# Kernel optimization log

Measured on AMD Instinct MI355X. Metric: run time of the kernel, lower is better.

The kernel has to match this reference:

```python
import jax, jax.numpy as jnp
import numpy as np

B, T = 64, 512
VOCAB = 1024
HID = [512, 512]
STATE = HID[0]          # 512
CELL_IN = 2 * STATE     # 1024 (emb || h)
CELL_OUT = STATE + VOCAB  # 1536
SKIP_DIM = sum(HID)     # 1024


def setup_inputs() -> dict:
    key = jax.random.key(0)
    ks = jax.random.split(key, 8)
    s = 0.02
    x = jax.random.randint(ks[0], (B, T), 0, VOCAB, dtype=jnp.int32)
    emb = jax.random.normal(ks[1], (VOCAB, STATE), dtype=jnp.float32) * s
    W0 = jax.random.normal(ks[2], (CELL_IN, HID[0]), dtype=jnp.float32) * s
    b0 = jnp.zeros((HID[0],), dtype=jnp.float32)
    W1 = jax.random.normal(ks[3], (HID[0], HID[1]), dtype=jnp.float32) * s
    b1 = jnp.zeros((HID[1],), dtype=jnp.float32)
    Wout = jax.random.normal(ks[4], (SKIP_DIM, CELL_OUT), dtype=jnp.float32) * s
    bout = jnp.zeros((CELL_OUT,), dtype=jnp.float32)
    return {"x": x, "emb": emb, "W0": W0, "b0": b0, "W1": W1, "b1": b1,
            "Wout": Wout, "bout": bout}


def reference(x, emb, W0, b0, W1, b1, Wout, bout):
    # embedding gather for all timesteps: [B, T, STATE] -> [T, B, STATE] for scan
    e = emb[x].transpose(1, 0, 2)

    def step(h, e_t):
        inp = jnp.concatenate([e_t, h], axis=-1)          # [B, 2*STATE]
        h0 = jax.nn.relu(inp @ W0 + b0)                   # [B, HID0]
        h1 = jax.nn.relu(h0 @ W1 + b1)                    # [B, HID1]
        cat = jnp.concatenate([h0, h1], axis=-1)          # skip connection
        cell_out = cat @ Wout + bout                      # [B, STATE+VOCAB]
        h_new = jax.nn.relu(cell_out[:, :STATE])
        logits = cell_out[:, STATE:]
        return h_new, logits

    h0 = jnp.zeros((x.shape[0], STATE), dtype=emb.dtype)
    _, logits = jax.lax.scan(step, h0, e)                 # logits: [T, B, VOCAB]
    return logits.transpose(1, 0, 2)                      # [B, T, VOCAB]
```

## Files before the change

### kernel.cpp

```cpp
#include <hip/hip_runtime.h>
#include <hip/hip_bf16.h>

typedef __attribute__((ext_vector_type(8))) short short8;
typedef __attribute__((ext_vector_type(4))) float f32x4;
typedef __attribute__((ext_vector_type(2))) unsigned long long u64x2;

#define MFMA16(a, b, c) __builtin_amdgcn_mfma_f32_16x16x32_bf16((a), (b), (c), 0, 0, 0)

#define B_ 64
#define T_ 512
#define STATE_ 512
#define NG 16
#define NGROUPS 4

#define CNT_OFF   0u
#define HBUF_OFF  24576u
#define CAT_OFF   155648u
#define W0F_OFF   67264512u
#define W1F_OFF   68313088u
#define WAF_OFF   68837376u
#define WBT_OFF   69885952u

__device__ __forceinline__ short f2bf(float f) {
  unsigned u = __float_as_uint(f);
  unsigned r = (u + 0x7fffu + ((u >> 16) & 1u)) >> 16;
  return (short)r;
}

__device__ __forceinline__ short8 ld8(const short* p) {
  union { u64x2 q; short8 s; } u;
  u.q.x = __hip_atomic_load((const unsigned long long*)p, __ATOMIC_RELAXED, __HIP_MEMORY_SCOPE_AGENT);
  u.q.y = __hip_atomic_load(((const unsigned long long*)p) + 1, __ATOMIC_RELAXED, __HIP_MEMORY_SCOPE_AGENT);
  return u.s;
}

__device__ __forceinline__ void st2(short* p, float v0, float v1) {
  unsigned pk = ((unsigned)(unsigned short)f2bf(v1) << 16) | (unsigned)(unsigned short)f2bf(v0);
  __hip_atomic_store((unsigned*)p, pk, __ATOMIC_RELAXED, __HIP_MEMORY_SCOPE_AGENT);
}

__global__ void pack_weights(const float* __restrict__ W0, const float* __restrict__ W1,
                             const float* __restrict__ Wout,
                             short* __restrict__ W0f, short* __restrict__ W1f,
                             short* __restrict__ Waf, short* __restrict__ WbT) {
  const int total = 524288 + 262144 + 524288 + 1048576;
  for (int i = blockIdx.x * blockDim.x + threadIdx.x; i < total; i += gridDim.x * blockDim.x) {
    if (i < 524288) {
      int j = i & 7, l = (i >> 3) & 63, rest = i >> 9;
      int s = rest & 31, cb = rest >> 5;
      int k = s * 32 + ((l >> 4) << 3) + j, n = (cb << 4) + (l & 15);
      W0f[i] = f2bf(W0[k * 512 + n]);
    } else if (i < 786432) {
      int ii = i - 524288;
      int j = ii & 7, l = (ii >> 3) & 63, rest = ii >> 9;
      int s = rest & 15, cb = rest >> 4;
      int k = s * 32 + ((l >> 4) << 3) + j, n = (cb << 4) + (l & 15);
      W1f[ii] = f2bf(W1[k * 512 + n]);
    } else if (i < 1310720) {
      int ii = i - 786432;
      int j = ii & 7, l = (ii >> 3) & 63, rest = ii >> 9;
      int s = rest & 31, cb = rest >> 5;
      int k = s * 32 + ((l >> 4) << 3) + j, n = (cb << 4) + (l & 15);
      Waf[ii] = f2bf(Wout[k * 1536 + n]);
    } else {
      int ii = i - 1310720;
      int v = ii >> 10, k = ii & 1023;
      WbT[ii] = f2bf(Wout[k * 1536 + 512 + v]);
    }
  }
}

__device__ __forceinline__ void group_barrier(unsigned* __restrict__ flags, int g, int m,
                                              unsigned tag) {
  __syncthreads();
  const int tid = threadIdx.x;
  if (tid == 0)
    __hip_atomic_store(&flags[(g << 4) + m], tag, __ATOMIC_RELEASE, __HIP_MEMORY_SCOPE_AGENT);
  if (tid < NG) {
    int spins = 0;
    while (__hip_atomic_load(&flags[(g << 4) + tid], __ATOMIC_RELAXED,
                             __HIP_MEMORY_SCOPE_AGENT) < tag) {
      if (++spins > (1 << 16)) break;
    }
  }
  __syncthreads();
}

__device__ __forceinline__ float rsum(const float* red, int rr, int col) {
  int o = ((col >> 4) << 8) + rr * 16 + (col & 15);
  return red[o] + red[o + 512] + red[o + 1024] + red[o + 1536];
}

__global__ __launch_bounds__(256, 1) void rnn_recur(
    const int* __restrict__ x, const float* __restrict__ emb,
    const float* __restrict__ b0, const float* __restrict__ b1,
    const float* __restrict__ bout,
    const short* __restrict__ W0f, const short* __restrict__ W1f,
    const short* __restrict__ Waf,
    short* __restrict__ cat, short* __restrict__ hbuf, unsigned* __restrict__ flags) {
  const int tid = threadIdx.x;
  const int l = tid & 63, w = tid >> 6;
  const int g = blockIdx.x >> 4, m = blockIdx.x & 15;
  const int rowbase = g << 4, colbase = m << 5;
  __shared__ float red[2048];

  short8 w0f[2][8], waL[2][4], waH[2][4], w1f[2][4];
#pragma unroll
  for (int tile = 0; tile < 2; ++tile) {
    int cb = m * 2 + tile;
#pragma unroll
    for (int s = 0; s < 8; ++s)
      w0f[tile][s] = *(const short8*)&W0f[((cb * 32 + w * 8 + s) * 64 + l) * 8];
#pragma unroll
    for (int s = 0; s < 4; ++s) {
      waL[tile][s] = *(const short8*)&Waf[((cb * 32 + w * 4 + s) * 64 + l) * 8];
      waH[tile][s] = *(const short8*)&Waf[((cb * 32 + 16 + w * 4 + s) * 64 + l) * 8];
      w1f[tile][s] = *(const short8*)&W1f[((cb * 16 + w * 4 + s) * 64 + l) * 8];
    }
  }

  const int cp = tid & 15, rr2 = tid >> 4;
  const float b0a = b0[colbase + 2 * cp],   b0b = b0[colbase + 2 * cp + 1];
  const float b1a = b1[colbase + 2 * cp],   b1b = b1[colbase + 2 * cp + 1];
  const float bOa = bout[colbase + 2 * cp], bOb = bout[colbase + 2 * cp + 1];

  const int myrow = rowbase + (l & 15);
  const int kgrp = (l >> 4) * 8;

  for (int t = 0; t < T_; ++t) {
    {
      f32x4 acc0 = {0.f, 0.f, 0.f, 0.f}, acc1 = {0.f, 0.f, 0.f, 0.f};
      if (w < 2) {
        int idx = x[myrow * T_ + t];
        const float* erow = emb + (long)idx * STATE_ + w * 256 + kgrp;
#pragma unroll
        for (int s = 0; s < 8; ++s) {
          const float* p = erow + s * 32;
          short8 a;
#pragma unroll
          for (int j = 0; j < 8; ++j) a[j] = f2bf(p[j]);
          acc0 = MFMA16(a, w0f[0][s], acc0);
          acc1 = MFMA16(a, w0f[1][s], acc1);
        }
      } else {
        const short* hrow = hbuf + ((t & 1) << 15) + (myrow << 9) + (w - 2) * 256 + kgrp;
#pragma unroll
        for (int s = 0; s < 8; ++s) {
          short8 a = ld8(hrow + s * 32);
          acc0 = MFMA16(a, w0f[0][s], acc0);
          acc1 = MFMA16(a, w0f[1][s], acc1);
        }
      }
#pragma unroll
      for (int j = 0; j < 4; ++j) {
        red[w * 512 +       ((l >> 4) * 4 + j) * 16 + (l & 15)] = acc0[j];
        red[w * 512 + 256 + ((l >> 4) * 4 + j) * 16 + (l & 15)] = acc1[j];
      }
      __syncthreads();
      float v0 = fmaxf(rsum(red, rr2, 2 * cp) + b0a, 0.f);
      float v1 = fmaxf(rsum(red, rr2, 2 * cp + 1) + b0b, 0.f);
      st2(&cat[(t * B_ + rowbase + rr2) * 1024 + colbase + 2 * cp], v0, v1);
    }
    group_barrier(flags, g, m, (unsigned)(t * 3 + 1));

    f32x4 accP0 = {0.f, 0.f, 0.f, 0.f}, accP1 = {0.f, 0.f, 0.f, 0.f};
    {
      f32x4 acc0 = {0.f, 0.f, 0.f, 0.f}, acc1 = {0.f, 0.f, 0.f, 0.f};
      const short* crow = cat + (t * B_ + myrow) * 1024 + w * 128 + kgrp;
#pragma unroll
      for (int s = 0; s < 4; ++s) {
        short8 a = ld8(crow + s * 32);
        acc0 = MFMA16(a, w1f[0][s], acc0);
        acc1 = MFMA16(a, w1f[1][s], acc1);
        accP0 = MFMA16(a, waL[0][s], accP0);
        accP1 = MFMA16(a, waL[1][s], accP1);
      }
#pragma unroll
      for (int j = 0; j < 4; ++j) {
        red[w * 512 +       ((l >> 4) * 4 + j) * 16 + (l & 15)] = acc0[j];
        red[w * 512 + 256 + ((l >> 4) * 4 + j) * 16 + (l & 15)] = acc1[j];
      }
      __syncthreads();
      float v0 = fmaxf(rsum(red, rr2, 2 * cp) + b1a, 0.f);
      float v1 = fmaxf(rsum(red, rr2, 2 * cp + 1) + b1b, 0.f);
      st2(&cat[(t * B_ + rowbase + rr2) * 1024 + 512 + colbase + 2 * cp], v0, v1);
    }
    if (t == T_ - 1) break;
    group_barrier(flags, g, m, (unsigned)(t * 3 + 2));

    {
      const short* crow = cat + (t * B_ + myrow) * 1024 + 512 + w * 128 + kgrp;
#pragma unroll
      for (int s = 0; s < 4; ++s) {
        short8 a = ld8(crow + s * 32);
        accP0 = MFMA16(a, waH[0][s], accP0);
        accP1 = MFMA16(a, waH[1][s], accP1);
      }
#pragma unroll
      for (int j = 0; j < 4; ++j) {
        red[w * 512 +       ((l >> 4) * 4 + j) * 16 + (l & 15)] = accP0[j];
        red[w * 512 + 256 + ((l >> 4) * 4 + j) * 16 + (l & 15)] = accP1[j];
      }
      __syncthreads();
      float v0 = fmaxf(rsum(red, rr2, 2 * cp) + bOa, 0.f);
      float v1 = fmaxf(rsum(red, rr2, 2 * cp + 1) + bOb, 0.f);
      st2(&hbuf[(((t + 1) & 1) << 15) + (rowbase + rr2) * 512 + colbase + 2 * cp], v0, v1);
    }
    group_barrier(flags, g, m, (unsigned)(t * 3 + 3));
  }
}

__global__ __launch_bounds__(256) void logits_gemm(const short* __restrict__ cat,
                                                   const short* __restrict__ WbT,
                                                   const float* __restrict__ bout,
                                                   float* __restrict__ out) {
  const int mbase = (blockIdx.x >> 3) * 128;
  const int vbase = (blockIdx.x & 7) * 128;
  __shared__ short sA[128 * 32];
  __shared__ short sB[128 * 32];
  const int tid = threadIdx.x, l = tid & 63, w = tid >> 6;
  const int wm = w & 1, wn = w >> 1;

  f32x4 acc[4][4];
#pragma unroll
  for (int i = 0; i < 4; ++i)
#pragma unroll
    for (int j = 0; j < 4; ++j) acc[i][j] = (f32x4){0.f, 0.f, 0.f, 0.f};

  for (int kb = 0; kb < 1024; kb += 32) {
    __syncthreads();
#pragma unroll
    for (int it = 0; it < 2; ++it) {
      int c = tid + 256 * it;
      int ml = c >> 2, ks = c & 3;
      *(short8*)&sA[ml * 32 + ks * 8] = *(const short8*)&cat[(mbase + ml) * 1024 + kb + ks * 8];
      *(short8*)&sB[ml * 32 + ks * 8] = *(const short8*)&WbT[(vbase + ml) * 1024 + kb + ks * 8];
    }
    __syncthreads();
    short8 af[4], bf[4];
#pragma unroll
    for (int fr = 0; fr < 4; ++fr)
      af[fr] = *(const short8*)&sA[(wm * 64 + fr * 16 + (l & 15)) * 32 + (l >> 4) * 8];
#pragma unroll
    for (int fc = 0; fc < 4; ++fc)
      bf[fc] = *(const short8*)&sB[(wn * 64 + fc * 16 + (l & 15)) * 32 + (l >> 4) * 8];
#pragma unroll
    for (int fr = 0; fr < 4; ++fr)
#pragma unroll
      for (int fc = 0; fc < 4; ++fc) acc[fr][fc] = MFMA16(af[fr], bf[fc], acc[fr][fc]);
  }

  float bb[4];
#pragma unroll
  for (int fc = 0; fc < 4; ++fc) bb[fc] = bout[512 + vbase + wn * 64 + fc * 16 + (l & 15)];

#pragma unroll
  for (int fr = 0; fr < 4; ++fr) {
#pragma unroll
    for (int fc = 0; fc < 4; ++fc) {
      int v = vbase + wn * 64 + fc * 16 + (l & 15);
#pragma unroll
      for (int j = 0; j < 4; ++j) {
        int mm = mbase + wm * 64 + fr * 16 + (l >> 4) * 4 + j;
        int b = mm & 63, tt = mm >> 6;
        out[((long)(b * T_ + tt)) * 1024 + v] = acc[fr][fc][j] + bb[fc];
      }
    }
  }
}

extern "C" void kernel_launch(void* const* d_in, const int* in_sizes, int n_in,
                              void* d_out, int out_size, void* d_ws, size_t ws_size,
                              hipStream_t stream) {
  const int*   x    = (const int*)d_in[0];
  const float* emb  = (const float*)d_in[1];
  const float* W0   = (const float*)d_in[2];
  const float* b0   = (const float*)d_in[3];
  const float* W1   = (const float*)d_in[4];
  const float* b1   = (const float*)d_in[5];
  const float* Wout = (const float*)d_in[6];
  const float* bout = (const float*)d_in[7];
  float* out = (float*)d_out;

  char* ws = (char*)d_ws;
  unsigned* flags = (unsigned*)(ws + CNT_OFF);
  short* hbuf = (short*)(ws + HBUF_OFF);
  short* cat  = (short*)(ws + CAT_OFF);
  short* W0f  = (short*)(ws + W0F_OFF);
  short* W1f  = (short*)(ws + W1F_OFF);
  short* Waf  = (short*)(ws + WAF_OFF);
  short* WbT  = (short*)(ws + WBT_OFF);

  hipMemsetAsync(ws, 0, HBUF_OFF + 131072u, stream);
  pack_weights<<<1024, 256, 0, stream>>>(W0, W1, Wout, W0f, W1f, Waf, WbT);
  rnn_recur<<<64, 256, 0, stream>>>(x, emb, b0, b1, bout, W0f, W1f, Waf, cat, hbuf, flags);
  logits_gemm<<<2048, 256, 0, stream>>>(cat, WbT, bout, out);
}
```

Baseline: 6.368 ms.

## Remap recurrent blocks onto XCDs with full-K per wave and per-XCD flag barriers

Each block now reads its XCC id at startup and claims a slot so that each group of 8 batch rows runs on 8 blocks sharing one XCD. Each wave owns a 16-column tile over the full K dimension, so the LDS cross-wave reduction and its syncthreads go away. Barriers become split signal/wait flags, and when a group fits on one XCD it uses plain loads and stores without cache invalidation. The embedding is pre-converted to bf16 and the token ids are staged in LDS. In exchange it holds far more weights in registers and depends on an XCC-placement rendezvous among all 64 blocks.

```diff
diff --git a/kernel.cpp b/kernel.cpp
--- a/kernel.cpp
+++ b/kernel.cpp
@@ -9,17 +9,16 @@
 
 #define B_ 64
 #define T_ 512
-#define STATE_ 512
-#define NG 16
-#define NGROUPS 4
-
-#define CNT_OFF   0u
-#define HBUF_OFF  24576u
-#define CAT_OFF   155648u
-#define W0F_OFF   67264512u
-#define W1F_OFF   68313088u
-#define WAF_OFF   68837376u
-#define WBT_OFF   69885952u
+
+#define ORG_OFF   0u
+#define FLAGS_OFF 1024u
+#define HBUF_OFF  4096u
+#define CAT_OFF   135168u
+#define W0F_OFF   67244032u
+#define W1F_OFF   68292608u
+#define WAF_OFF   68816896u
+#define WBT_OFF   69865472u
+#define EMBF_OFF  71962624u
 
 __device__ __forceinline__ short f2bf(float f) {
   unsigned u = __float_as_uint(f);
@@ -34,16 +33,22 @@
   return u.s;
 }
 
-__device__ __forceinline__ void st2(short* p, float v0, float v1) {
-  unsigned pk = ((unsigned)(unsigned short)f2bf(v1) << 16) | (unsigned)(unsigned short)f2bf(v0);
-  __hip_atomic_store((unsigned*)p, pk, __ATOMIC_RELAXED, __HIP_MEMORY_SCOPE_AGENT);
+__device__ __forceinline__ void st_bf(short* p, float v, int fast) {
+  unsigned short b = (unsigned short)f2bf(v);
+  if (fast) {
+    *p = (short)b;
+  } else {
+    unsigned vv = b;
+    asm volatile("global_store_short %0, %1, off sc0 sc1" :: "v"(p), "v"(vv) : "memory");
+  }
 }
 
 __global__ void pack_weights(const float* __restrict__ W0, const float* __restrict__ W1,
-                             const float* __restrict__ Wout,
+                             const float* __restrict__ Wout, const float* __restrict__ emb,
                              short* __restrict__ W0f, short* __restrict__ W1f,
-                             short* __restrict__ Waf, short* __restrict__ WbT) {
-  const int total = 524288 + 262144 + 524288 + 1048576;
+                             short* __restrict__ Waf, short* __restrict__ WbT,
+                             short* __restrict__ embf) {
+  const int total = 524288 + 262144 + 524288 + 1048576 + 524288;
   for (int i = blockIdx.x * blockDim.x + threadIdx.x; i < total; i += gridDim.x * blockDim.x) {
     if (i < 524288) {
       int j = i & 7, l = (i >> 3) & 63, rest = i >> 9;
@@ -62,151 +67,185 @@
       int s = rest & 31, cb = rest >> 5;
       int k = s * 32 + ((l >> 4) << 3) + j, n = (cb << 4) + (l & 15);
       Waf[ii] = f2bf(Wout[k * 1536 + n]);
-    } else {
+    } else if (i < 2359296) {
       int ii = i - 1310720;
       int v = ii >> 10, k = ii & 1023;
       WbT[ii] = f2bf(Wout[k * 1536 + 512 + v]);
-    }
-  }
-}
-
-__device__ __forceinline__ void group_barrier(unsigned* __restrict__ flags, int g, int m,
-                                              unsigned tag) {
+    } else {
+      int ii = i - 2359296;
+      embf[ii] = f2bf(emb[ii]);
+    }
+  }
+}
+
+__device__ __forceinline__ void wait_tag(unsigned* gf, unsigned tag, int inv) {
+  if (threadIdx.x < 8) {
+    int spins = 0;
+    while (__hip_atomic_load(&gf[threadIdx.x], __ATOMIC_RELAXED, __HIP_MEMORY_SCOPE_AGENT) < tag) {
+      if (++spins > (1 << 22)) break;
+    }
+  }
   __syncthreads();
-  const int tid = threadIdx.x;
-  if (tid == 0)
-    __hip_atomic_store(&flags[(g << 4) + m], tag, __ATOMIC_RELEASE, __HIP_MEMORY_SCOPE_AGENT);
-  if (tid < NG) {
-    int spins = 0;
-    while (__hip_atomic_load(&flags[(g << 4) + tid], __ATOMIC_RELAXED,
-                             __HIP_MEMORY_SCOPE_AGENT) < tag) {
-      if (++spins > (1 << 16)) break;
-    }
-  }
+  if (inv) asm volatile("buffer_inv" ::: "memory");
+}
+
+__device__ __forceinline__ void signal_tag(unsigned* gf, int mb, unsigned tag) {
   __syncthreads();
-}
-
-__device__ __forceinline__ float rsum(const float* red, int rr, int col) {
-  int o = ((col >> 4) << 8) + rr * 16 + (col & 15);
-  return red[o] + red[o + 512] + red[o + 1024] + red[o + 1536];
+  if (threadIdx.x == 0) {
+    asm volatile("" ::: "memory");
+    __hip_atomic_store(&gf[mb], tag, __ATOMIC_RELAXED, __HIP_MEMORY_SCOPE_AGENT);
+  }
 }
 
 __global__ __launch_bounds__(256, 1) void rnn_recur(
-    const int* __restrict__ x, const float* __restrict__ emb,
-    const float* __restrict__ b0, const float* __restrict__ b1,
-    const float* __restrict__ bout,
-    const short* __restrict__ W0f, const short* __restrict__ W1f,
-    const short* __restrict__ Waf,
-    short* __restrict__ cat, short* __restrict__ hbuf, unsigned* __restrict__ flags) {
+    const int* __restrict__ x,
+    const float* __restrict__ b0, const float* __restrict__ b1, const float* __restrict__ bout,
+    const short* __restrict__ W0f, const short* __restrict__ W1f, const short* __restrict__ Waf,
+    const short* __restrict__ embf,
+    short* __restrict__ cat, short* __restrict__ hbuf,
+    unsigned* __restrict__ org, unsigned* __restrict__ flagsbase) {
   const int tid = threadIdx.x;
   const int l = tid & 63, w = tid >> 6;
-  const int g = blockIdx.x >> 4, m = blockIdx.x & 15;
-  const int rowbase = g << 4, colbase = m << 5;
-  __shared__ float red[2048];
-
-  short8 w0f[2][8], waL[2][4], waH[2][4], w1f[2][4];
-#pragma unroll
-  for (int tile = 0; tile < 2; ++tile) {
-    int cb = m * 2 + tile;
-#pragma unroll
-    for (int s = 0; s < 8; ++s)
-      w0f[tile][s] = *(const short8*)&W0f[((cb * 32 + w * 8 + s) * 64 + l) * 8];
-#pragma unroll
-    for (int s = 0; s < 4; ++s) {
-      waL[tile][s] = *(const short8*)&Waf[((cb * 32 + w * 4 + s) * 64 + l) * 8];
-      waH[tile][s] = *(const short8*)&Waf[((cb * 32 + 16 + w * 4 + s) * 64 + l) * 8];
-      w1f[tile][s] = *(const short8*)&W1f[((cb * 16 + w * 4 + s) * 64 + l) * 8];
-    }
-  }
-
-  const int cp = tid & 15, rr2 = tid >> 4;
-  const float b0a = b0[colbase + 2 * cp],   b0b = b0[colbase + 2 * cp + 1];
-  const float b1a = b1[colbase + 2 * cp],   b1b = b1[colbase + 2 * cp + 1];
-  const float bOa = bout[colbase + 2 * cp], bOb = bout[colbase + 2 * cp + 1];
-
-  const int myrow = rowbase + (l & 15);
-  const int kgrp = (l >> 4) * 8;
+  __shared__ int s_g, s_m, s_fast;
+  __shared__ int x_lds[8][512];
+
+  if (tid == 0) {
+    unsigned xcc = __builtin_amdgcn_s_getreg(20 | (31 << 11)) & 7u;
+    int slot = (int)__hip_atomic_fetch_add(&org[xcc], 1u, __ATOMIC_RELAXED, __HIP_MEMORY_SCOPE_AGENT);
+    int sp = -1;
+    if (slot >= 8)
+      sp = (int)__hip_atomic_fetch_add(&org[8], 1u, __ATOMIC_RELAXED, __HIP_MEMORY_SCOPE_AGENT);
+    __hip_atomic_fetch_add(&org[9], 1u, __ATOMIC_RELEASE, __HIP_MEMORY_SCOPE_AGENT);
+    int spins = 0;
+    while (__hip_atomic_load(&org[9], __ATOMIC_ACQUIRE, __HIP_MEMORY_SCOPE_AGENT) < 64u) {
+      if (++spins > (1 << 22)) break;
+    }
+    unsigned c[8];
+    for (int i = 0; i < 8; ++i)
+      c[i] = __hip_atomic_load(&org[i], __ATOMIC_RELAXED, __HIP_MEMORY_SCOPE_AGENT);
+    int g, mb;
+    if (sp < 0) { g = (int)xcc; mb = slot; }
+    else {
+      int want = sp, acc = 0; g = 0; mb = 0;
+      for (int xx = 0; xx < 8; ++xx) {
+        int d = (c[xx] < 8u) ? (8 - (int)c[xx]) : 0;
+        if (want < acc + d) { g = xx; mb = (int)c[xx] + (want - acc); break; }
+        acc += d;
+      }
+    }
+    s_g = g; s_m = mb; s_fast = (c[g] >= 8u) ? 1 : 0;
+  }
+  __syncthreads();
+  const int g = s_g, mb = s_m, fast = s_fast;
+
+  for (int i = tid; i < 8 * 512; i += 256)
+    x_lds[i >> 9][i & 511] = x[(g * 8 + (i >> 9)) * T_ + (i & 511)];
+
+  const int cb = mb * 4 + w;
+  short8 w0f[32], w1f[16], waf[32];
+#pragma unroll
+  for (int s = 0; s < 32; ++s) w0f[s] = *(const short8*)&W0f[((cb * 32 + s) * 64 + l) * 8];
+#pragma unroll
+  for (int s = 0; s < 16; ++s) w1f[s] = *(const short8*)&W1f[((cb * 16 + s) * 64 + l) * 8];
+#pragma unroll
+  for (int s = 0; s < 32; ++s) waf[s] = *(const short8*)&Waf[((cb * 32 + s) * 64 + l) * 8];
+
+  const int col512 = cb * 16 + (l & 15);
+  const int lrow = (l & 15) & 7;
+  const int kofs = (l >> 4) * 8;
+  const float b0v = b0[col512], b1v = b1[col512], bOv = bout[col512];
+  unsigned* gf = flagsbase + g * 16;
+  __syncthreads();
 
   for (int t = 0; t < T_; ++t) {
-    {
-      f32x4 acc0 = {0.f, 0.f, 0.f, 0.f}, acc1 = {0.f, 0.f, 0.f, 0.f};
-      if (w < 2) {
-        int idx = x[myrow * T_ + t];
-        const float* erow = emb + (long)idx * STATE_ + w * 256 + kgrp;
-#pragma unroll
-        for (int s = 0; s < 8; ++s) {
-          const float* p = erow + s * 32;
-          short8 a;
-#pragma unroll
-          for (int j = 0; j < 8; ++j) a[j] = f2bf(p[j]);
-          acc0 = MFMA16(a, w0f[0][s], acc0);
-          acc1 = MFMA16(a, w0f[1][s], acc1);
+    f32x4 accA = {0.f, 0.f, 0.f, 0.f}, accB = {0.f, 0.f, 0.f, 0.f};
+    {
+      int idx = x_lds[lrow][t];
+      const short* ep = embf + idx * 512 + kofs;
+#pragma unroll
+      for (int s = 0; s < 16; s += 2) {
+        short8 a0 = *(const short8*)(ep + s * 32);
+        short8 a1 = *(const short8*)(ep + s * 32 + 32);
+        accA = MFMA16(a0, w0f[s], accA);
+        accB = MFMA16(a1, w0f[s + 1], accB);
+      }
+    }
+    wait_tag(gf, (unsigned)(3 * t), fast);
+    {
+      const short* hp = hbuf + ((t & 1) << 15) + ((g * 8 + lrow) << 9) + kofs;
+      if (fast) {
+#pragma unroll
+        for (int s = 0; s < 16; s += 2) {
+          short8 a0 = *(const short8*)(hp + s * 32);
+          short8 a1 = *(const short8*)(hp + s * 32 + 32);
+          accA = MFMA16(a0, w0f[16 + s], accA);
+          accB = MFMA16(a1, w0f[17 + s], accB);
         }
       } else {
-        const short* hrow = hbuf + ((t & 1) << 15) + (myrow << 9) + (w - 2) * 256 + kgrp;
-#pragma unroll
-        for (int s = 0; s < 8; ++s) {
-          short8 a = ld8(hrow + s * 32);
-          acc0 = MFMA16(a, w0f[0][s], acc0);
-          acc1 = MFMA16(a, w0f[1][s], acc1);
+#pragma unroll
+        for (int s = 0; s < 16; s += 2) {
+          short8 a0 = ld8(hp + s * 32);
+          short8 a1 = ld8(hp + s * 32 + 32);
+          accA = MFMA16(a0, w0f[16 + s], accA);
+          accB = MFMA16(a1, w0f[17 + s], accB);
         }
       }
+    }
+    {
+      f32x4 hv = accA + accB;
+      short* cp = cat + (t * B_ + g * 8) * 1024 + col512;
 #pragma unroll
       for (int j = 0; j < 4; ++j) {
-        red[w * 512 +       ((l >> 4) * 4 + j) * 16 + (l & 15)] = acc0[j];
-        red[w * 512 + 256 + ((l >> 4) * 4 + j) * 16 + (l & 15)] = acc1[j];
-      }
-      __syncthreads();
-      float v0 = fmaxf(rsum(red, rr2, 2 * cp) + b0a, 0.f);
-      float v1 = fmaxf(rsum(red, rr2, 2 * cp + 1) + b0b, 0.f);
-      st2(&cat[(t * B_ + rowbase + rr2) * 1024 + colbase + 2 * cp], v0, v1);
-    }
-    group_barrier(flags, g, m, (unsigned)(t * 3 + 1));
-
-    f32x4 accP0 = {0.f, 0.f, 0.f, 0.f}, accP1 = {0.f, 0.f, 0.f, 0.f};
-    {
-      f32x4 acc0 = {0.f, 0.f, 0.f, 0.f}, acc1 = {0.f, 0.f, 0.f, 0.f};
-      const short* crow = cat + (t * B_ + myrow) * 1024 + w * 128 + kgrp;
-#pragma unroll
-      for (int s = 0; s < 4; ++s) {
-        short8 a = ld8(crow + s * 32);
-        acc0 = MFMA16(a, w1f[0][s], acc0);
-        acc1 = MFMA16(a, w1f[1][s], acc1);
-        accP0 = MFMA16(a, waL[0][s], accP0);
-        accP1 = MFMA16(a, waL[1][s], accP1);
-      }
+        int r = (l >> 4) * 4 + j;
+        if (r < 8) st_bf(cp + r * 1024, fmaxf(hv[j] + b0v, 0.f), fast);
+      }
+    }
+    signal_tag(gf, mb, (unsigned)(3 * t + 1));
+
+    wait_tag(gf, (unsigned)(3 * t + 1), 0);
+    f32x4 pA = {0.f, 0.f, 0.f, 0.f}, pB = {0.f, 0.f, 0.f, 0.f};
+    {
+      f32x4 hA = {0.f, 0.f, 0.f, 0.f}, hB = {0.f, 0.f, 0.f, 0.f};
+      const short* c0 = cat + (t * B_ + g * 8 + lrow) * 1024 + kofs;
+#pragma unroll
+      for (int s = 0; s < 16; s += 2) {
+        short8 a0 = *(const short8*)(c0 + s * 32);
+        short8 a1 = *(const short8*)(c0 + s * 32 + 32);
+        hA = MFMA16(a0, w1f[s], hA);
+        hB = MFMA16(a1, w1f[s + 1], hB);
+        pA = MFMA16(a0, waf[s], pA);
+        pB = MFMA16(a1, waf[s + 1], pB);
+      }
+      f32x4 hv = hA + hB;
+      short* cp = cat + (t * B_ + g * 8) * 1024 + 512 + col512;
 #pragma unroll
       for (int j = 0; j < 4; ++j) {
-        red[w * 512 +       ((l >> 4) * 4 + j) * 16 + (l & 15)] = acc0[j];
-        red[w * 512 + 256 + ((l >> 4) * 4 + j) * 16 + (l & 15)] = acc1[j];
-      }
-      __syncthreads();
-      float v0 = fmaxf(rsum(red, rr2, 2 * cp) + b1a, 0.f);
-      float v1 = fmaxf(rsum(red, rr2, 2 * cp + 1) + b1b, 0.f);
-      st2(&cat[(t * B_ + rowbase + rr2) * 1024 + 512 + colbase + 2 * cp], v0, v1);
+        int r = (l >> 4) * 4 + j;
+        if (r < 8) st_bf(cp + r * 1024, fmaxf(hv[j] + b1v, 0.f), fast);
+      }
     }
     if (t == T_ - 1) break;
-    group_barrier(flags, g, m, (unsigned)(t * 3 + 2));
-
-    {
-      const short* crow = cat + (t * B_ + myrow) * 1024 + 512 + w * 128 + kgrp;
-#pragma unroll
-      for (int s = 0; s < 4; ++s) {
-        short8 a = ld8(crow + s * 32);
-        accP0 = MFMA16(a, waH[0][s], accP0);
-        accP1 = MFMA16(a, waH[1][s], accP1);
-      }
+    signal_tag(gf, mb, (unsigned)(3 * t + 2));
+
+    wait_tag(gf, (unsigned)(3 * t + 2), 0);
+    {
+      const short* c1 = cat + (t * B_ + g * 8 + lrow) * 1024 + 512 + kofs;
+#pragma unroll
+      for (int s = 0; s < 16; s += 2) {
+        short8 a0 = *(const short8*)(c1 + s * 32);
+        short8 a1 = *(const short8*)(c1 + s * 32 + 32);
+        pA = MFMA16(a0, waf[16 + s], pA);
+        pB = MFMA16(a1, waf[17 + s], pB);
+      }
+      f32x4 hv = pA + pB;
+      short* hq = hbuf + (((t + 1) & 1) << 15) + (g * 8) * 512 + col512;
 #pragma unroll
       for (int j = 0; j < 4; ++j) {
-        red[w * 512 +       ((l >> 4) * 4 + j) * 16 + (l & 15)] = accP0[j];
-        red[w * 512 + 256 + ((l >> 4) * 4 + j) * 16 + (l & 15)] = accP1[j];
-      }
-      __syncthreads();
-      float v0 = fmaxf(rsum(red, rr2, 2 * cp) + bOa, 0.f);
-      float v1 = fmaxf(rsum(red, rr2, 2 * cp + 1) + bOb, 0.f);
-      st2(&hbuf[(((t + 1) & 1) << 15) + (rowbase + rr2) * 512 + colbase + 2 * cp], v0, v1);
-    }
-    group_barrier(flags, g, m, (unsigned)(t * 3 + 3));
+        int r = (l >> 4) * 4 + j;
+        if (r < 8) st_bf(hq + r * 512, fmaxf(hv[j] + bOv, 0.f), fast);
+      }
+    }
+    signal_tag(gf, mb, (unsigned)(3 * t + 3));
   }
 }
 
@@ -283,16 +322,18 @@
   float* out = (float*)d_out;
 
   char* ws = (char*)d_ws;
-  unsigned* flags = (unsigned*)(ws + CNT_OFF);
+  unsigned* org   = (unsigned*)(ws + ORG_OFF);
+  unsigned* flags = (unsigned*)(ws + FLAGS_OFF);
   short* hbuf = (short*)(ws + HBUF_OFF);
   short* cat  = (short*)(ws + CAT_OFF);
   short* W0f  = (short*)(ws + W0F_OFF);
   short* W1f  = (short*)(ws + W1F_OFF);
   short* Waf  = (short*)(ws + WAF_OFF);
   short* WbT  = (short*)(ws + WBT_OFF);
+  short* embf = (short*)(ws + EMBF_OFF);
 
   hipMemsetAsync(ws, 0, HBUF_OFF + 131072u, stream);
-  pack_weights<<<1024, 256, 0, stream>>>(W0, W1, Wout, W0f, W1f, Waf, WbT);
-  rnn_recur<<<64, 256, 0, stream>>>(x, emb, b0, b1, bout, W0f, W1f, Waf, cat, hbuf, flags);
+  pack_weights<<<1024, 256, 0, stream>>>(W0, W1, Wout, emb, W0f, W1f, Waf, WbT, embf);
+  rnn_recur<<<64, 256, 0, stream>>>(x, b0, b1, bout, W0f, W1f, Waf, embf, cat, hbuf, org, flags);
   logits_gemm<<<2048, 256, 0, stream>>>(cat, WbT, bout, out);
 }
```

Result: no change. 6.426 ms (+0.9%).

## Precompute embedding projection and restructure recurrence to redundant-compute per batch group

Applied to the files above, without the earlier changes.

Adds an eprime kernel that precomputes emb @ W0[:512] for the whole vocabulary, so each step only gathers a row instead of multiplying the embedding half. The recurrence now runs 16 blocks of 1024 threads. Each block of four computes h0 and h1 redundantly in LDS from the full h state, then splits only the state-output projection, so there is one cross-block flag sync per step instead of three. This cuts inter-block synchronisation and global round-trips on the serial critical path. In exchange it duplicates the h0/h1 work in every block, uses fewer CUs, and Epr stays in fp32, which changes the rounding point of the embedding term.

```diff
diff --git a/kernel.cpp b/kernel.cpp
--- a/kernel.cpp
+++ b/kernel.cpp
@@ -9,17 +9,15 @@
 
 #define B_ 64
 #define T_ 512
-#define STATE_ 512
-#define NG 16
-#define NGROUPS 4
-
-#define CNT_OFF   0u
-#define HBUF_OFF  24576u
-#define CAT_OFF   155648u
-#define W0F_OFF   67264512u
-#define W1F_OFF   68313088u
-#define WAF_OFF   68837376u
-#define WBT_OFF   69885952u
+
+#define FLG_OFF  0u
+#define HNEW_OFF 1024u
+#define CAT_OFF  66560u
+#define W0F_OFF  67175424u
+#define W1F_OFF  67699712u
+#define WAF_OFF  68224000u
+#define WBT_OFF  69272576u
+#define EPR_OFF  71369728u
 
 __device__ __forceinline__ short f2bf(float f) {
   unsigned u = __float_as_uint(f);
@@ -34,179 +32,271 @@
   return u.s;
 }
 
-__device__ __forceinline__ void st2(short* p, float v0, float v1) {
-  unsigned pk = ((unsigned)(unsigned short)f2bf(v1) << 16) | (unsigned)(unsigned short)f2bf(v0);
-  __hip_atomic_store((unsigned*)p, pk, __ATOMIC_RELAXED, __HIP_MEMORY_SCOPE_AGENT);
-}
-
 __global__ void pack_weights(const float* __restrict__ W0, const float* __restrict__ W1,
                              const float* __restrict__ Wout,
                              short* __restrict__ W0f, short* __restrict__ W1f,
                              short* __restrict__ Waf, short* __restrict__ WbT) {
-  const int total = 524288 + 262144 + 524288 + 1048576;
+  const int total = 262144 + 262144 + 524288 + 1048576;
   for (int i = blockIdx.x * blockDim.x + threadIdx.x; i < total; i += gridDim.x * blockDim.x) {
-    if (i < 524288) {
+    if (i < 262144) {
       int j = i & 7, l = (i >> 3) & 63, rest = i >> 9;
-      int s = rest & 31, cb = rest >> 5;
+      int s = rest & 15, cb = rest >> 4;
       int k = s * 32 + ((l >> 4) << 3) + j, n = (cb << 4) + (l & 15);
-      W0f[i] = f2bf(W0[k * 512 + n]);
-    } else if (i < 786432) {
-      int ii = i - 524288;
+      W0f[i] = f2bf(W0[(512 + k) * 512 + n]);
+    } else if (i < 524288) {
+      int ii = i - 262144;
       int j = ii & 7, l = (ii >> 3) & 63, rest = ii >> 9;
       int s = rest & 15, cb = rest >> 4;
       int k = s * 32 + ((l >> 4) << 3) + j, n = (cb << 4) + (l & 15);
       W1f[ii] = f2bf(W1[k * 512 + n]);
-    } else if (i < 1310720) {
-      int ii = i - 786432;
+    } else if (i < 1048576) {
+      int ii = i - 524288;
       int j = ii & 7, l = (ii >> 3) & 63, rest = ii >> 9;
       int s = rest & 31, cb = rest >> 5;
       int k = s * 32 + ((l >> 4) << 3) + j, n = (cb << 4) + (l & 15);
       Waf[ii] = f2bf(Wout[k * 1536 + n]);
     } else {
-      int ii = i - 1310720;
-      int v = ii >> 10, k = ii & 1023;
-      WbT[ii] = f2bf(Wout[k * 1536 + 512 + v]);
-    }
-  }
-}
-
-__device__ __forceinline__ void group_barrier(unsigned* __restrict__ flags, int g, int m,
-                                              unsigned tag) {
+      int ii = i - 1048576;
+      int v = ii >> 10, kk = ii & 1023;
+      WbT[ii] = f2bf(Wout[kk * 1536 + 512 + v]);
+    }
+  }
+}
+
+__global__ __launch_bounds__(256) void eprime(const float* __restrict__ emb,
+                                              const float* __restrict__ W0,
+                                              float* __restrict__ Epr) {
+  __shared__ float eL[16][512];
+  const int v0 = blockIdx.x * 16, tid = threadIdx.x;
+  for (int i = tid; i < 16 * 512; i += 256)
+    eL[i >> 9][i & 511] = emb[(v0 + (i >> 9)) * 512 + (i & 511)];
   __syncthreads();
-  const int tid = threadIdx.x;
-  if (tid == 0)
-    __hip_atomic_store(&flags[(g << 4) + m], tag, __ATOMIC_RELEASE, __HIP_MEMORY_SCOPE_AGENT);
-  if (tid < NG) {
-    int spins = 0;
-    while (__hip_atomic_load(&flags[(g << 4) + tid], __ATOMIC_RELAXED,
-                             __HIP_MEMORY_SCOPE_AGENT) < tag) {
-      if (++spins > (1 << 16)) break;
-    }
-  }
-  __syncthreads();
-}
-
-__device__ __forceinline__ float rsum(const float* red, int rr, int col) {
-  int o = ((col >> 4) << 8) + rr * 16 + (col & 15);
-  return red[o] + red[o + 512] + red[o + 1024] + red[o + 1536];
-}
-
-__global__ __launch_bounds__(256, 1) void rnn_recur(
-    const int* __restrict__ x, const float* __restrict__ emb,
-    const float* __restrict__ b0, const float* __restrict__ b1,
-    const float* __restrict__ bout,
-    const short* __restrict__ W0f, const short* __restrict__ W1f,
-    const short* __restrict__ Waf,
-    short* __restrict__ cat, short* __restrict__ hbuf, unsigned* __restrict__ flags) {
-  const int tid = threadIdx.x;
-  const int l = tid & 63, w = tid >> 6;
-  const int g = blockIdx.x >> 4, m = blockIdx.x & 15;
-  const int rowbase = g << 4, colbase = m << 5;
-  __shared__ float red[2048];
-
-  short8 w0f[2][8], waL[2][4], waH[2][4], w1f[2][4];
-#pragma unroll
-  for (int tile = 0; tile < 2; ++tile) {
-    int cb = m * 2 + tile;
-#pragma unroll
-    for (int s = 0; s < 8; ++s)
-      w0f[tile][s] = *(const short8*)&W0f[((cb * 32 + w * 8 + s) * 64 + l) * 8];
-#pragma unroll
-    for (int s = 0; s < 4; ++s) {
-      waL[tile][s] = *(const short8*)&Waf[((cb * 32 + w * 4 + s) * 64 + l) * 8];
-      waH[tile][s] = *(const short8*)&Waf[((cb * 32 + 16 + w * 4 + s) * 64 + l) * 8];
-      w1f[tile][s] = *(const short8*)&W1f[((cb * 16 + w * 4 + s) * 64 + l) * 8];
-    }
-  }
-
-  const int cp = tid & 15, rr2 = tid >> 4;
-  const float b0a = b0[colbase + 2 * cp],   b0b = b0[colbase + 2 * cp + 1];
-  const float b1a = b1[colbase + 2 * cp],   b1b = b1[colbase + 2 * cp + 1];
-  const float bOa = bout[colbase + 2 * cp], bOb = bout[colbase + 2 * cp + 1];
-
-  const int myrow = rowbase + (l & 15);
-  const int kgrp = (l >> 4) * 8;
+  float acc[32];
+#pragma unroll
+  for (int v = 0; v < 32; ++v) acc[v] = 0.f;
+#pragma unroll 4
+  for (int k = 0; k < 512; ++k) {
+    float wa = W0[k * 512 + tid];
+    float wb = W0[k * 512 + 256 + tid];
+#pragma unroll
+    for (int v = 0; v < 16; ++v) {
+      float e = eL[v][k];
+      acc[2 * v]     = fmaf(e, wa, acc[2 * v]);
+      acc[2 * v + 1] = fmaf(e, wb, acc[2 * v + 1]);
+    }
+  }
+#pragma unroll
+  for (int v = 0; v < 16; ++v) {
+    Epr[(v0 + v) * 512 + tid]       = acc[2 * v];
+    Epr[(v0 + v) * 512 + 256 + tid] = acc[2 * v + 1];
+  }
+}
+
+__global__ __launch_bounds__(1024, 1) void rnn_recur(
+    const int* __restrict__ x,
+    const float* __restrict__ b0, const float* __restrict__ b1, const float* __restrict__ bout,
+    const short* __restrict__ W0f, const short* __restrict__ W1f, const short* __restrict__ Waf,
+    const float* __restrict__ Epr,
+    short* __restrict__ cat, unsigned* __restrict__ hnewG, unsigned* __restrict__ flags) {
+  const int g = blockIdx.x >> 2, m = blockIdx.x & 3;
+  const int tid = threadIdx.x, l = tid & 63, w = tid >> 6;
+  const int ks = w >> 3, cs = w & 7;
+  const int kq = w >> 2, cw = w & 3;
+  const int q = l >> 4, r16 = l & 15;
+
+  __shared__ short hst[16 * 512];
+  __shared__ short h0s[16 * 512];
+  __shared__ short h1s[16 * 512];
+  __shared__ float part[8][4][16][17];
+  __shared__ float part3[3][4][2][16][17];
+  __shared__ short pub[16 * 128];
+
+  short8 w0r[4][8], w1r[4][8], war[2][8];
+#pragma unroll
+  for (int cb = 0; cb < 4; ++cb) {
+    int cbg = cs * 4 + cb;
+#pragma unroll
+    for (int si = 0; si < 8; ++si) {
+      int s = ks * 8 + si;
+      w0r[cb][si] = *(const short8*)&W0f[((cbg * 16 + s) * 64 + l) * 8];
+      w1r[cb][si] = *(const short8*)&W1f[((cbg * 16 + s) * 64 + l) * 8];
+    }
+  }
+#pragma unroll
+  for (int cb = 0; cb < 2; ++cb) {
+    int cbg = m * 8 + cw * 2 + cb;
+#pragma unroll
+    for (int si = 0; si < 8; ++si) {
+      int s = kq * 8 + si;
+      war[cb][si] = *(const short8*)&Waf[((cbg * 32 + s) * 64 + l) * 8];
+    }
+  }
+
+  float b0v[4], b1v[4];
+#pragma unroll
+  for (int cb = 0; cb < 4; ++cb) {
+    int c = (cs * 4 + cb) * 16 + r16;
+    b0v[cb] = b0[c]; b1v[cb] = b1[c];
+  }
+  float bov[2];
+#pragma unroll
+  for (int cb = 0; cb < 2; ++cb) bov[cb] = bout[(m * 8 + cw * 2 + cb) * 16 + r16];
+
+  float epf[16];
+  if (ks == 1) {
+#pragma unroll
+    for (int j = 0; j < 4; ++j) {
+      int xi = x[(g * 16 + q * 4 + j) * T_ + 0];
+#pragma unroll
+      for (int cb = 0; cb < 4; ++cb)
+        epf[cb * 4 + j] = Epr[xi * 512 + (cs * 4 + cb) * 16 + r16];
+    }
+  }
 
   for (int t = 0; t < T_; ++t) {
+    if (tid < 4) {
+      int spins = 0;
+      while (__hip_atomic_load(&flags[g * 16 + tid], __ATOMIC_RELAXED,
+                               __HIP_MEMORY_SCOPE_AGENT) < (unsigned)t) {
+        if (++spins > (1 << 22)) break;
+      }
+    }
+    __syncthreads();
     {
-      f32x4 acc0 = {0.f, 0.f, 0.f, 0.f}, acc1 = {0.f, 0.f, 0.f, 0.f};
-      if (w < 2) {
-        int idx = x[myrow * T_ + t];
-        const float* erow = emb + (long)idx * STATE_ + w * 256 + kgrp;
-#pragma unroll
-        for (int s = 0; s < 8; ++s) {
-          const float* p = erow + s * 32;
-          short8 a;
-#pragma unroll
-          for (int j = 0; j < 8; ++j) a[j] = f2bf(p[j]);
-          acc0 = MFMA16(a, w0f[0][s], acc0);
-          acc1 = MFMA16(a, w0f[1][s], acc1);
+      short8 hv = ld8((const short*)hnewG + g * 8192 + tid * 8);
+      int rr = tid >> 6, cbyte = (tid & 63) * 16;
+      *(short8*)&hst[rr * 512 + ((cbyte ^ ((rr & 7) << 6)) >> 1)] = hv;
+    }
+    __syncthreads();
+
+    {
+      f32x4 acc[4];
+#pragma unroll
+      for (int cb = 0; cb < 4; ++cb) acc[cb] = (f32x4){0.f, 0.f, 0.f, 0.f};
+#pragma unroll
+      for (int si = 0; si < 8; ++si) {
+        int kbyte = (ks * 256 + si * 32 + q * 8) * 2;
+        short8 af = *(const short8*)&hst[r16 * 512 + ((kbyte ^ ((r16 & 7) << 6)) >> 1)];
+#pragma unroll
+        for (int cb = 0; cb < 4; ++cb) acc[cb] = MFMA16(af, w0r[cb][si], acc[cb]);
+      }
+      if (ks == 0) {
+#pragma unroll
+        for (int cb = 0; cb < 4; ++cb)
+#pragma unroll
+          for (int j = 0; j < 4; ++j) part[cs][cb][q * 4 + j][r16] = acc[cb][j];
+      }
+      __syncthreads();
+      if (ks == 1) {
+#pragma unroll
+        for (int cb = 0; cb < 4; ++cb) {
+          int c = (cs * 4 + cb) * 16 + r16;
+#pragma unroll
+          for (int j = 0; j < 4; ++j) {
+            int rr = q * 4 + j;
+            float v = acc[cb][j] + part[cs][cb][rr][r16] + epf[cb * 4 + j] + b0v[cb];
+            short bf = f2bf(fmaxf(v, 0.f));
+            h0s[rr * 512 + (((c * 2) ^ ((rr & 7) << 6)) >> 1)] = bf;
+            if (m == 0) cat[(t * B_ + g * 16 + rr) * 1024 + c] = bf;
+          }
         }
-      } else {
-        const short* hrow = hbuf + ((t & 1) << 15) + (myrow << 9) + (w - 2) * 256 + kgrp;
-#pragma unroll
-        for (int s = 0; s < 8; ++s) {
-          short8 a = ld8(hrow + s * 32);
-          acc0 = MFMA16(a, w0f[0][s], acc0);
-          acc1 = MFMA16(a, w0f[1][s], acc1);
+      }
+      __syncthreads();
+    }
+
+    {
+      f32x4 acc[4];
+#pragma unroll
+      for (int cb = 0; cb < 4; ++cb) acc[cb] = (f32x4){0.f, 0.f, 0.f, 0.f};
+#pragma unroll
+      for (int si = 0; si < 8; ++si) {
+        int kbyte = (ks * 256 + si * 32 + q * 8) * 2;
+        short8 af = *(const short8*)&h0s[r16 * 512 + ((kbyte ^ ((r16 & 7) << 6)) >> 1)];
+#pragma unroll
+        for (int cb = 0; cb < 4; ++cb) acc[cb] = MFMA16(af, w1r[cb][si], acc[cb]);
+      }
+      if (ks == 0) {
+#pragma unroll
+        for (int cb = 0; cb < 4; ++cb)
+#pragma unroll
+          for (int j = 0; j < 4; ++j) part[cs][cb][q * 4 + j][r16] = acc[cb][j];
+      }
+      __syncthreads();
+      if (ks == 1) {
+#pragma unroll
+        for (int cb = 0; cb < 4; ++cb) {
+          int c = (cs * 4 + cb) * 16 + r16;
+#pragma unroll
+          for (int j = 0; j < 4; ++j) {
+            int rr = q * 4 + j;
+            float v = acc[cb][j] + part[cs][cb][rr][r16] + b1v[cb];
+            short bf = f2bf(fmaxf(v, 0.f));
+            h1s[rr * 512 + (((c * 2) ^ ((rr & 7) << 6)) >> 1)] = bf;
+            if (m == 1) cat[(t * B_ + g * 16 + rr) * 1024 + 512 + c] = bf;
+          }
         }
-      }
-#pragma unroll
-      for (int j = 0; j < 4; ++j) {
-        red[w * 512 +       ((l >> 4) * 4 + j) * 16 + (l & 15)] = acc0[j];
-        red[w * 512 + 256 + ((l >> 4) * 4 + j) * 16 + (l & 15)] = acc1[j];
-      }
-      __syncthreads();
-      float v0 = fmaxf(rsum(red, rr2, 2 * cp) + b0a, 0.f);
-      float v1 = fmaxf(rsum(red, rr2, 2 * cp + 1) + b0b, 0.f);
-      st2(&cat[(t * B_ + rowbase + rr2) * 1024 + colbase + 2 * cp], v0, v1);
-    }
-    group_barrier(flags, g, m, (unsigned)(t * 3 + 1));
-
-    f32x4 accP0 = {0.f, 0.f, 0.f, 0.f}, accP1 = {0.f, 0.f, 0.f, 0.f};
+        if (t + 1 < T_) {
+#pragma unroll
+          for (int j = 0; j < 4; ++j) {
+            int xi = x[(g * 16 + q * 4 + j) * T_ + t + 1];
+#pragma unroll
+            for (int cb = 0; cb < 4; ++cb)
+              epf[cb * 4 + j] = Epr[xi * 512 + (cs * 4 + cb) * 16 + r16];
+          }
+        }
+      }
+      __syncthreads();
+    }
+
+    if (t == T_ - 1) break;
+
     {
-      f32x4 acc0 = {0.f, 0.f, 0.f, 0.f}, acc1 = {0.f, 0.f, 0.f, 0.f};
-      const short* crow = cat + (t * B_ + myrow) * 1024 + w * 128 + kgrp;
-#pragma unroll
-      for (int s = 0; s < 4; ++s) {
-        short8 a = ld8(crow + s * 32);
-        acc0 = MFMA16(a, w1f[0][s], acc0);
-        acc1 = MFMA16(a, w1f[1][s], acc1);
-        accP0 = MFMA16(a, waL[0][s], accP0);
-        accP1 = MFMA16(a, waL[1][s], accP1);
-      }
-#pragma unroll
-      for (int j = 0; j < 4; ++j) {
-        red[w * 512 +       ((l >> 4) * 4 + j) * 16 + (l & 15)] = acc0[j];
-        red[w * 512 + 256 + ((l >> 4) * 4 + j) * 16 + (l & 15)] = acc1[j];
-      }
-      __syncthreads();
-      float v0 = fmaxf(rsum(red, rr2, 2 * cp) + b1a, 0.f);
-      float v1 = fmaxf(rsum(red, rr2, 2 * cp + 1) + b1b, 0.f);
-      st2(&cat[(t * B_ + rowbase + rr2) * 1024 + 512 + colbase + 2 * cp], v0, v1);
-    }
-    if (t == T_ - 1) break;
-    group_barrier(flags, g, m, (unsigned)(t * 3 + 2));
-
-    {
-      const short* crow = cat + (t * B_ + myrow) * 1024 + 512 + w * 128 + kgrp;
-#pragma unroll
-      for (int s = 0; s < 4; ++s) {
-        short8 a = ld8(crow + s * 32);
-        accP0 = MFMA16(a, waH[0][s], accP0);
-        accP1 = MFMA16(a, waH[1][s], accP1);
-      }
-#pragma unroll
-      for (int j = 0; j < 4; ++j) {
-        red[w * 512 +       ((l >> 4) * 4 + j) * 16 + (l & 15)] = accP0[j];
-        red[w * 512 + 256 + ((l >> 4) * 4 + j) * 16 + (l & 15)] = accP1[j];
-      }
-      __syncthreads();
-      float v0 = fmaxf(rsum(red, rr2, 2 * cp) + bOa, 0.f);
-      float v1 = fmaxf(rsum(red, rr2, 2 * cp + 1) + bOb, 0.f);
-      st2(&hbuf[(((t + 1) & 1) << 15) + (rowbase + rr2) * 512 + colbase + 2 * cp], v0, v1);
-    }
-    group_barrier(flags, g, m, (unsigned)(t * 3 + 3));
+      f32x4 a3[2];
+#pragma unroll
+      for (int cb = 0; cb < 2; ++cb) a3[cb] = (f32x4){0.f, 0.f, 0.f, 0.f};
+      const short* src = (kq < 2) ? h0s : h1s;
+      int kb = (kq & 1) * 256;
+#pragma unroll
+      for (int si = 0; si < 8; ++si) {
+        int kbyte = (kb + si * 32 + q * 8) * 2;
+        short8 af = *(const short8*)&src[r16 * 512 + ((kbyte ^ ((r16 & 7) << 6)) >> 1)];
+#pragma unroll
+        for (int cb = 0; cb < 2; ++cb) a3[cb] = MFMA16(af, war[cb][si], a3[cb]);
+      }
+      if (kq < 3) {
+#pragma unroll
+        for (int cb = 0; cb < 2; ++cb)
+#pragma unroll
+          for (int j = 0; j < 4; ++j) part3[kq][cw][cb][q * 4 + j][r16] = a3[cb][j];
+      }
+      __syncthreads();
+      if (kq == 3) {
+#pragma unroll
+        for (int cb = 0; cb < 2; ++cb) {
+          int lc = (cw * 2 + cb) * 16 + r16;
+#pragma unroll
+          for (int j = 0; j < 4; ++j) {
+            int rr = q * 4 + j;
+            float v = a3[cb][j] + part3[0][cw][cb][rr][r16] + part3[1][cw][cb][rr][r16] +
+                      part3[2][cw][cb][rr][r16] + bov[cb];
+            pub[rr * 128 + lc] = f2bf(fmaxf(v, 0.f));
+          }
+        }
+      }
+      __syncthreads();
+      {
+        int rr = tid >> 6, c2 = tid & 63;
+        unsigned word = ((const unsigned*)pub)[rr * 64 + c2];
+        __hip_atomic_store(&hnewG[g * 4096 + rr * 256 + m * 64 + c2], word,
+                           __ATOMIC_RELAXED, __HIP_MEMORY_SCOPE_AGENT);
+      }
+      __syncthreads();
+      if (tid == 0) {
+        asm volatile("s_waitcnt vmcnt(0)" ::: "memory");
+        __hip_atomic_store(&flags[g * 16 + m], (unsigned)(t + 1),
+                           __ATOMIC_RELEASE, __HIP_MEMORY_SCOPE_AGENT);
+      }
+    }
   }
 }
 
@@ -232,9 +322,9 @@
 #pragma unroll
     for (int it = 0; it < 2; ++it) {
       int c = tid + 256 * it;
-      int ml = c >> 2, ks = c & 3;
-      *(short8*)&sA[ml * 32 + ks * 8] = *(const short8*)&cat[(mbase + ml) * 1024 + kb + ks * 8];
-      *(short8*)&sB[ml * 32 + ks * 8] = *(const short8*)&WbT[(vbase + ml) * 1024 + kb + ks * 8];
+      int ml = c >> 2, kss = c & 3;
+      *(short8*)&sA[ml * 32 + kss * 8] = *(const short8*)&cat[(mbase + ml) * 1024 + kb + kss * 8];
+      *(short8*)&sB[ml * 32 + kss * 8] = *(const short8*)&WbT[(vbase + ml) * 1024 + kb + kss * 8];
     }
     __syncthreads();
     short8 af[4], bf[4];
@@ -283,16 +373,18 @@
   float* out = (float*)d_out;
 
   char* ws = (char*)d_ws;
-  unsigned* flags = (unsigned*)(ws + CNT_OFF);
-  short* hbuf = (short*)(ws + HBUF_OFF);
+  unsigned* flags = (unsigned*)(ws + FLG_OFF);
+  unsigned* hnewG = (unsigned*)(ws + HNEW_OFF);
   short* cat  = (short*)(ws + CAT_OFF);
   short* W0f  = (short*)(ws + W0F_OFF);
   short* W1f  = (short*)(ws + W1F_OFF);
   short* Waf  = (short*)(ws + WAF_OFF);
   short* WbT  = (short*)(ws + WBT_OFF);
-
-  hipMemsetAsync(ws, 0, HBUF_OFF + 131072u, stream);
+  float* Epr  = (float*)(ws + EPR_OFF);
+
+  hipMemsetAsync(ws, 0, CAT_OFF, stream);
   pack_weights<<<1024, 256, 0, stream>>>(W0, W1, Wout, W0f, W1f, Waf, WbT);
-  rnn_recur<<<64, 256, 0, stream>>>(x, emb, b0, b1, bout, W0f, W1f, Waf, cat, hbuf, flags);
+  eprime<<<64, 256, 0, stream>>>(emb, W0, Epr);
+  rnn_recur<<<16, 1024, 0, stream>>>(x, b0, b1, bout, W0f, W1f, Waf, Epr, cat, hnewG, flags);
   logits_gemm<<<2048, 256, 0, stream>>>(cat, WbT, bout, out);
 }
```

Result: slower. 21.58 ms (+238.9%).
